# Kernel optimization log

Measured on AMD Instinct MI355X. Metric: run time of the kernel, lower is better.

The kernel has to match this reference:

```python
import jax, jax.numpy as jnp
import numpy as np

N_HEAD = 8


def setup_inputs() -> dict:
    key = jax.random.key(0)
    ks = jax.random.split(key, 8)
    v, b, c, h, w = 8, 4, 512, 16, 16
    s = 1.0 / np.sqrt(c).astype(np.float32)
    return {
        "q": jax.random.normal(ks[0], (v, b, c, h, w), jnp.float32),
        "kv": jax.random.normal(ks[1], (v, b, c, h, w), jnp.float32),
        "Wq": jax.random.normal(ks[2], (c, c), jnp.float32) * s,
        "bq": jnp.zeros((c,), jnp.float32),
        "Wkv": jax.random.normal(ks[3], (c, 2 * c), jnp.float32) * s,
        "bkv": jnp.zeros((2 * c,), jnp.float32),
        "Wp": jax.random.normal(ks[4], (c, c), jnp.float32) * s,
        "bp": jnp.zeros((c,), jnp.float32),
    }


def reference(q, kv, Wq, bq, Wkv, bkv, Wp, bp):
    vi, bi, ci, hi, wi = q.shape
    hw = hi * wi
    T = vi * hw
    hd = ci // N_HEAD

    # rearrange 'v b c h w -> b (v h w) c'
    xq = q.transpose(1, 0, 3, 4, 2).reshape(bi, T, ci)
    xkv = kv.transpose(1, 0, 3, 4, 2).reshape(bi, T, ci)

    qp = xq @ Wq + bq                      # [b, T, c]
    k, v_ = jnp.split(xkv @ Wkv + bkv, 2, axis=-1)

    def heads(x):
        return x.reshape(bi, T, N_HEAD, hd).transpose(0, 2, 1, 3)  # [b,h,T,d]

    qh, kh, vh = heads(qp), heads(k), heads(v_)

    att = jnp.einsum('bhqd,bhkd->bhqk', qh, kh) * (1.0 / np.sqrt(hd).astype(np.float32))

    # block-causal mask: query block (size h*w) may attend to key blocks <= its own
    blocks = jnp.arange(T) // hw
    mask = blocks[:, None] >= blocks[None, :]
    att = jnp.where(mask, att, -jnp.inf)
    att = jax.nn.softmax(att, axis=-1)

    y = jnp.einsum('bhqk,bhkd->bhqd', att, vh)
    y = y.transpose(0, 2, 1, 3).reshape(bi, T, ci)
    y = y @ Wp + bp

    # rearrange 'b (v h w) c -> v b c h w'
    return y.reshape(bi, vi, hi, wi, ci).transpose(1, 0, 4, 2, 3)
```

## Files before the change

### kernel.cpp

```cpp
#include <hip/hip_runtime.h>
#include <hip/hip_bf16.h>
#include <cmath>

typedef unsigned short u16;
typedef __attribute__((ext_vector_type(8))) short s8v;
typedef __attribute__((ext_vector_type(4))) float f4v;
typedef __attribute__((ext_vector_type(2))) float f2v;
typedef __attribute__((ext_vector_type(4))) unsigned int u32x4;
typedef __attribute__((ext_vector_type(4))) unsigned short u16x4;

#define MFMA(a,b,c) __builtin_amdgcn_mfma_f32_16x16x32_bf16((a),(b),(c),0,0,0)

__device__ __forceinline__ float bf2f(u16 u) {
    union { float f; unsigned i; } x; x.i = ((unsigned)u) << 16; return x.f;
}
__device__ __forceinline__ u16 f2bf(float f) {
    union { float f; unsigned i; } x; x.f = f;
    unsigned r = x.i + 0x7FFFu + ((x.i >> 16) & 1u);
    return (u16)(r >> 16);
}
__device__ __forceinline__ unsigned cvtpk(float lo, float hi) {
    unsigned r;
    asm("v_cvt_pk_bf16_f32 %0, %1, %2" : "=v"(r) : "v"(lo), "v"(hi));
    return r;
}
__device__ __forceinline__ void gload_lds16(const void* g, void* l) {
    __builtin_amdgcn_global_load_lds(
        (const __attribute__((address_space(1))) unsigned int*)g,
        (__attribute__((address_space(3))) unsigned int*)l, 16, 0, 0);
}
__device__ __forceinline__ int swb(int row, int colb) {
    return row * 128 + (colb ^ ((((row >> 4) ^ row) & 7) << 4));
}

__constant__ int CPER[8]  = {1,1,2,2,3,3,4,4};
__constant__ int POFF[17] = {0,1,2,3,4,6,8,10,12,15,18,21,24,28,32,36,40};

__global__ __launch_bounds__(256, 3)
void qkv_proj(const float* __restrict__ q, const float* __restrict__ kv,
              const float* __restrict__ Wq, const float* __restrict__ bq,
              const float* __restrict__ Wkv, const float* __restrict__ bkv,
              u16* __restrict__ QH, u16* __restrict__ KH, u16* __restrict__ VT)
{
    __shared__ __align__(16) u16 Tl[2][128 * 64];

    const int bid = blockIdx.x;
    const int x = bid & 7, i = bid >> 3;
    const int mt = x + 8 * (i / 12);
    const int nt = i % 12;
    const int m0 = mt << 7, n0 = nt << 7;

    const int tid  = threadIdx.x;
    const int lane = tid & 63;
    const int w    = tid >> 6;
    const int wr = (w >> 1) * 64, wc = (w & 1) * 64;
    const int cl = lane & 15, rl = lane >> 4;

    const int bb  = m0 >> 11;
    const int t0  = m0 & 2047;
    const int vv  = t0 >> 8;
    const int hw0 = t0 & 255;

    const float* Abase = ((nt < 4) ? q : kv) + (size_t)(vv * 4 + bb) * 131072 + hw0;

    const float* W; const float* bias; int NW, wn0, dn0; u16* dst;
    if (nt < 4)      { W = Wq;  bias = bq;  NW = 512;  wn0 = n0;       dn0 = n0;        dst = QH; }
    else if (nt < 8) { W = Wkv; bias = bkv; NW = 1024; wn0 = n0 - 512; dn0 = n0 - 512;  dst = KH; }
    else             { W = Wkv; bias = bkv; NW = 1024; wn0 = n0 - 512; dn0 = n0 - 1024; dst = VT; }

    const float oscale = (nt < 4) ? 0.18033688011f : 1.0f;

    f4v acc[4][4] = {};
    f2v la0[8], lb0[8], la1[8], lb1[8];

    const int mh = tid & 63;
    const int kb = tid >> 6;

#define QKV_LOAD(dA, dB, k0_) do {                                           \
        const float* gA = Abase + (size_t)((k0_) + kb * 8) * 256 + mh * 2;   \
        const float* gB = W + (size_t)((k0_) + kb * 8) * NW + wn0 + mh * 2;  \
        _Pragma("unroll")                                                    \
        for (int j = 0; j < 8; ++j) {                                        \
            dA[j] = *reinterpret_cast<const f2v*>(gA + j * 256);             \
            dB[j] = *reinterpret_cast<const f2v*>(gB + (size_t)j * NW);      \
        }                                                                    \
    } while (0)

#define QKV_WRITE(bufi, sA, sB) do {                                         \
        _Pragma("unroll")                                                    \
        for (int e = 0; e < 2; ++e) {                                        \
            u32x4 pa, pb;                                                    \
            _Pragma("unroll")                                                \
            for (int jj = 0; jj < 4; ++jj) {                                 \
                pa[jj] = cvtpk(sA[jj * 2][e], sA[jj * 2 + 1][e]);            \
                pb[jj] = cvtpk(sB[jj * 2][e], sB[jj * 2 + 1][e]);            \
            }                                                                \
            *(u32x4*)((char*)&Tl[bufi][0] + swb(mh * 2 + e, kb * 16)) = pa;  \
            *(u32x4*)((char*)&Tl[bufi][0] + swb(mh * 2 + e, 64 + kb * 16)) = pb; \
        }                                                                    \
    } while (0)

#define QKV_MFMA(bufi) do {                                                  \
        s8v af[4], bf[4];                                                    \
        _Pragma("unroll")                                                    \
        for (int mi = 0; mi < 4; ++mi)                                       \
            af[mi] = *(const s8v*)((const char*)&Tl[bufi][0]                 \
                                   + swb(wr + mi * 16 + cl, rl * 16));       \
        _Pragma("unroll")                                                    \
        for (int ni = 0; ni < 4; ++ni)                                       \
            bf[ni] = *(const s8v*)((const char*)&Tl[bufi][0]                 \
                                   + swb(wc + ni * 16 + cl, 64 + rl * 16));  \
        _Pragma("unroll")                                                    \
        for (int mi = 0; mi < 4; ++mi)                                       \
            _Pragma("unroll")                                                \
            for (int ni = 0; ni < 4; ++ni)                                   \
                acc[mi][ni] = MFMA(af[mi], bf[ni], acc[mi][ni]);             \
    } while (0)

    QKV_LOAD(la0, lb0, 0);
    QKV_WRITE(0, la0, lb0);
    QKV_LOAD(la1, lb1, 32);
    __syncthreads();

    #pragma unroll
    for (int it = 0; it < 8; ++it) {
        const int t = it * 2;
        QKV_WRITE(1, la1, lb1);
        if (t + 2 < 16) QKV_LOAD(la0, lb0, (t + 2) * 32);
        QKV_MFMA(0);
        __syncthreads();
        if (t + 2 < 16) QKV_WRITE(0, la0, lb0);
        if (t + 3 < 16) QKV_LOAD(la1, lb1, (t + 3) * 32);
        QKV_MFMA(1);
        __syncthreads();
    }
#undef QKV_LOAD
#undef QKV_WRITE
#undef QKV_MFMA

    if (nt < 8) {
        #pragma unroll
        for (int ni = 0; ni < 4; ++ni) {
            const int nl   = wc + ni * 16 + cl;
            const float bv = bias[wn0 + nl];
            const int cout = dn0 + nl;
            const int hh = cout >> 6, dd = cout & 63;
            const size_t obase = ((size_t)(bb * 8 + hh) * 2048) * 64 + dd;
            #pragma unroll
            for (int mi = 0; mi < 4; ++mi)
                #pragma unroll
                for (int r = 0; r < 4; ++r) {
                    const int m = m0 + wr + mi * 16 + rl * 4 + r;
                    const int t = m & 2047;
                    dst[obase + (size_t)t * 64] = f2bf((acc[mi][ni][r] + bv) * oscale);
                }
        }
    } else {
        #pragma unroll
        for (int ni = 0; ni < 4; ++ni) {
            const int nl   = wc + ni * 16 + cl;
            const float bv = bias[wn0 + nl];
            const int cout = dn0 + nl;
            const int hh = cout >> 6, dd = cout & 63;
            const size_t obase = ((size_t)(bb * 8 + hh) * 64 + dd) * 2048;
            #pragma unroll
            for (int mi = 0; mi < 4; ++mi) {
                const int m = m0 + wr + mi * 16 + rl * 4;
                const int t = m & 2047;
                u16x4 pk;
                #pragma unroll
                for (int r = 0; r < 4; ++r) pk[r] = f2bf(acc[mi][ni][r] + bv);
                *reinterpret_cast<u16x4*>(dst + obase + t) = pk;
            }
        }
    }
}

__global__ __launch_bounds__(256, 4)
void attn_part(const u16* __restrict__ QH, const u16* __restrict__ KH,
               const u16* __restrict__ VT,
               u16* __restrict__ Opart, float* __restrict__ ML)
{
    __shared__ __align__(16) u16 Kl[2][4096];
    __shared__ __align__(16) u16 Vl[2][4096];
    __shared__ u16 Pl[4][16][36];

    const int wg = blockIdx.x;
    const int bh = wg & 31;
    const int s  = 39 - (wg >> 5);
    int p = 0;
    #pragma unroll
    for (int i = 0; i < 15; ++i) p += (s >= POFF[i + 1]) ? 1 : 0;
    const int c  = s - POFF[p];
    const int qb = p >> 1;
    const int kstart = c * 512;
    const int nk = min(512, (qb + 1) * 256 - kstart);
    const int nt64 = nk >> 6;

    const int tid = threadIdx.x, lane = tid & 63, w = tid >> 6;
    const int cl = lane & 15, rl = lane >> 4;

    const u16* Qb = QH + (size_t)bh * 131072;
    const u16* Kb = KH + (size_t)bh * 131072;
    const u16* Vb = VT + (size_t)bh * 131072;

    const int qrow0 = p * 128 + w * 32;

    s8v qf[2][2];
    #pragma unroll
    for (int mi = 0; mi < 2; ++mi)
        #pragma unroll
        for (int kf = 0; kf < 2; ++kf)
            qf[mi][kf] = *reinterpret_cast<const s8v*>(
                Qb + (size_t)(qrow0 + mi * 16 + cl) * 64 + kf * 32 + rl * 8);

    unsigned kofs[2], vofs[2];
    #pragma unroll
    for (int i = 0; i < 2; ++i) {
        const int f = w * 128 + i * 64 + lane;
        const int row = f >> 3;
        kofs[i] = row * 128 + (((f & 7) * 16) ^ ((row & 7) << 4));
        vofs[i] = row * 4096 + (((f & 7) * 16) ^ ((row & 7) << 4));
    }

#define ISSUE(bufi, kb0_) do {                                               \
        const char* kG = (const char*)Kb + (size_t)(kb0_) * 128;             \
        const char* vG = (const char*)Vb + (size_t)(kb0_) * 2;               \
        char* kL = (char*)&Kl[bufi][0] + w * 2048;                           \
        char* vL = (char*)&Vl[bufi][0] + w * 2048;                           \
        _Pragma("unroll")                                                    \
        for (int i_ = 0; i_ < 2; ++i_) {                                     \
            gload_lds16(kG + kofs[i_], kL + i_ * 1024);                      \
            gload_lds16(vG + vofs[i_], vL + i_ * 1024);                      \
        }                                                                    \
    } while (0)

    f4v o[2][4] = {};
    float lp[8] = {0.f, 0.f, 0.f, 0.f, 0.f, 0.f, 0.f, 0.f};

    ISSUE(0, kstart);

    for (int kt = 0; kt < nt64; ++kt) {
        asm volatile("s_waitcnt vmcnt(0)" ::: "memory");
        __builtin_amdgcn_sched_barrier(0);
        __syncthreads();
        if (kt + 1 < nt64) ISSUE((kt + 1) & 1, kstart + (kt + 1) * 64);

        const char* Kbase = (const char*)&Kl[kt & 1][0];
        const char* Vbase = (const char*)&Vl[kt & 1][0];

        f4v sc[2][4] = {};
        #pragma unroll
        for (int ni = 0; ni < 4; ++ni)
            #pragma unroll
            for (int kf = 0; kf < 2; ++kf) {
                const int row = ni * 16 + cl;
                s8v kfr = *reinterpret_cast<const s8v*>(
                    Kbase + row * 128 + ((kf * 64 + rl * 16) ^ ((row & 7) << 4)));
                sc[0][ni] = MFMA(qf[0][kf], kfr, sc[0][ni]);
                sc[1][ni] = MFMA(qf[1][kf], kfr, sc[1][ni]);
            }

        #pragma unroll
        for (int mi = 0; mi < 2; ++mi)
            #pragma unroll
            for (int ni = 0; ni < 4; ++ni)
                #pragma unroll
                for (int r = 0; r < 4; ++r)
                    sc[mi][ni][r] = exp2f(sc[mi][ni][r]);
        #pragma unroll
        for (int mi = 0; mi < 2; ++mi)
            #pragma unroll
            for (int r = 0; r < 4; ++r)
                lp[mi * 4 + r] += sc[mi][0][r] + sc[mi][1][r]
                                + sc[mi][2][r] + sc[mi][3][r];

        #pragma unroll
        for (int kw = 0; kw < 2; ++kw) {
            s8v pf0, pf1;
            #pragma unroll
            for (int jj = 0; jj < 2; ++jj) {
                const int ni = kw * 2 + jj;
                const unsigned w0 = cvtpk(sc[0][ni][0], sc[0][ni][1]);
                const unsigned w1 = cvtpk(sc[0][ni][2], sc[0][ni][3]);
                const int col = jj * 16 + cl;
                Pl[w][rl * 4 + 0][col] = (u16)w0;
                Pl[w][rl * 4 + 1][col] = (u16)(w0 >> 16);
                Pl[w][rl * 4 + 2][col] = (u16)w1;
                Pl[w][rl * 4 + 3][col] = (u16)(w1 >> 16);
            }
            pf0 = *reinterpret_cast<const s8v*>(&Pl[w][cl][rl * 8]);
            #pragma unroll
            for (int jj = 0; jj < 2; ++jj) {
                const int ni = kw * 2 + jj;
                const unsigned w0 = cvtpk(sc[1][ni][0], sc[1][ni][1]);
                const unsigned w1 = cvtpk(sc[1][ni][2], sc[1][ni][3]);
                const int col = jj * 16 + cl;
                Pl[w][rl * 4 + 0][col] = (u16)w0;
                Pl[w][rl * 4 + 1][col] = (u16)(w0 >> 16);
                Pl[w][rl * 4 + 2][col] = (u16)w1;
                Pl[w][rl * 4 + 3][col] = (u16)(w1 >> 16);
            }
            pf1 = *reinterpret_cast<const s8v*>(&Pl[w][cl][rl * 8]);
            #pragma unroll
            for (int di = 0; di < 4; ++di) {
                const int row = di * 16 + cl;
                s8v vf = *reinterpret_cast<const s8v*>(
                    Vbase + row * 128 + ((kw * 64 + rl * 16) ^ ((row & 7) << 4)));
                o[0][di] = MFMA(pf0, vf, o[0][di]);
                o[1][di] = MFMA(pf1, vf, o[1][di]);
            }
        }
    }
#undef ISSUE

    const int slot = bh * 40 + POFF[p] + c;
    #pragma unroll
    for (int mi = 0; mi < 2; ++mi)
        #pragma unroll
        for (int r = 0; r < 4; ++r) {
            const int idx = mi * 4 + r;
            float ls = lp[idx];
            ls += __shfl_xor(ls, 1);
            ls += __shfl_xor(ls, 2);
            ls += __shfl_xor(ls, 4);
            ls += __shfl_xor(ls, 8);
            const float inv = 1.f / ls;
            const int rloc = w * 32 + mi * 16 + rl * 4 + r;
            if (cl == 0) ML[(size_t)slot * 128 + rloc] = ls;
            #pragma unroll
            for (int di = 0; di < 4; ++di)
                Opart[(size_t)slot * 8192 + rloc * 64 + di * 16 + cl] =
                    f2bf(o[mi][di][r] * inv);
        }
}

__global__ __launch_bounds__(256)
void attn_combine(const u16* __restrict__ Opart, const float* __restrict__ ML,
                  u16* __restrict__ YH)
{
    const int wg = blockIdx.x;
    const int bh = wg & 31;
    const int p  = wg >> 5;
    const int b = bh >> 3, h = bh & 7;
    const int nc = CPER[p >> 1];
    const int sb = bh * 40 + POFF[p];

    const int t = threadIdx.x;
    const int rloc = t >> 1;
    const int dh = (t & 1) * 32;

    float lc[4], L = 0.f;
    for (int c = 0; c < nc; ++c) {
        lc[c] = ML[(size_t)(sb + c) * 128 + rloc];
        L += lc[c];
    }
    const float invL = 1.f / L;
    float wgt[4];
    for (int c = 0; c < nc; ++c) wgt[c] = lc[c] * invL;

    f4v a[8] = {};
    for (int c = 0; c < nc; ++c) {
        const float wv = wgt[c];
        #pragma unroll
        for (int u = 0; u < 4; ++u) {
            s8v vv = *reinterpret_cast<const s8v*>(
                &Opart[(size_t)(sb + c) * 8192 + rloc * 64 + dh + u * 8]);
            #pragma unroll
            for (int e = 0; e < 4; ++e) a[u * 2][e]     += wv * bf2f((u16)vv[e]);
            #pragma unroll
            for (int e = 0; e < 4; ++e) a[u * 2 + 1][e] += wv * bf2f((u16)vv[e + 4]);
        }
    }

    const size_t ybase = ((size_t)b * 2048 + p * 128 + rloc) * 512 + h * 64 + dh;
    #pragma unroll
    for (int u = 0; u < 4; ++u) {
        s8v ov;
        #pragma unroll
        for (int e = 0; e < 4; ++e) ov[e]     = (short)f2bf(a[u * 2][e]);
        #pragma unroll
        for (int e = 0; e < 4; ++e) ov[e + 4] = (short)f2bf(a[u * 2 + 1][e]);
        *reinterpret_cast<s8v*>(YH + ybase + u * 8) = ov;
    }
}

__global__ __launch_bounds__(256)
void out_proj(const u16* __restrict__ YH, const float* __restrict__ Wp,
              const float* __restrict__ bp, float* __restrict__ out)
{
    __shared__ __align__(16) u16 Al[2][128 * 64];
    __shared__ u16 Bl[2][128][40];

    const int bid = blockIdx.x;
    const int x = bid & 7, i = bid >> 3;
    const int mt = x + 8 * (i >> 2);
    const int ct = i & 3;
    const int c0 = ct << 7, m0 = mt << 7;

    const int tid = threadIdx.x, lane = tid & 63, w = tid >> 6;
    const int wr = (w >> 1) * 64, wc = (w & 1) * 64;
    const int cl = lane & 15, rl = lane >> 4;

    f4v acc[4][4] = {};
    f2v wa0[8], wa1[8];
    s8v sy0[2], sy1[2];

    const int mh = tid & 63;
    const int kb = tid >> 6;
    const int br = tid >> 2;
    const int bq4 = (tid & 3) * 8;

#define OP_LOAD(dA, dY, k0_) do {                                            \
        const float* gA = Wp + (size_t)((k0_) + kb * 8) * 512 + c0 + mh * 2; \
        _Pragma("unroll")                                                    \
        for (int j = 0; j < 8; ++j)                                          \
            dA[j] = *reinterpret_cast<const f2v*>(gA + j * 512);             \
        _Pragma("unroll")                                                    \
        for (int it = 0; it < 2; ++it)                                       \
            dY[it] = *reinterpret_cast<const s8v*>(                          \
                YH + (size_t)(m0 + br + it * 64) * 512 + (k0_) + bq4);       \
    } while (0)

#define OP_WRITE(bufi, sA, sY) do {                                          \
        _Pragma("unroll")                                                    \
        for (int e = 0; e < 2; ++e) {                                        \
            u32x4 pa;                                                        \
            _Pragma("unroll")                                                \
            for (int jj = 0; jj < 4; ++jj)                                   \
                pa[jj] = cvtpk(sA[jj * 2][e], sA[jj * 2 + 1][e]);            \
            *(u32x4*)((char*)&Al[bufi][0] + swb(mh * 2 + e, kb * 16)) = pa;  \
        }                                                                    \
        _Pragma("unroll")                                                    \
        for (int it = 0; it < 2; ++it)                                       \
            *reinterpret_cast<s8v*>(&Bl[bufi][br + it * 64][bq4]) = sY[it];  \
    } while (0)

#define OP_MFMA(bufi) do {                                                   \
        s8v af[4], bfr[4];                                                   \
        _Pragma("unroll")                                                    \
        for (int mi = 0; mi < 4; ++mi)                                       \
            af[mi] = *(const s8v*)((const char*)&Al[bufi][0]                 \
                                   + swb(wr + mi * 16 + cl, rl * 16));       \
        _Pragma("unroll")                                                    \
        for (int ni = 0; ni < 4; ++ni)                                       \
            bfr[ni] = *reinterpret_cast<const s8v*>(                         \
                &Bl[bufi][wc + ni * 16 + cl][rl * 8]);                       \
        _Pragma("unroll")                                                    \
        for (int mi = 0; mi < 4; ++mi)                                       \
            _Pragma("unroll")                                                \
            for (int ni = 0; ni < 4; ++ni)                                   \
                acc[mi][ni] = MFMA(af[mi], bfr[ni], acc[mi][ni]);            \
    } while (0)

    OP_LOAD(wa0, sy0, 0);
    OP_WRITE(0, wa0, sy0);
    OP_LOAD(wa1, sy1, 32);
    __syncthreads();

    #pragma unroll
    for (int it = 0; it < 8; ++it) {
        const int t = it * 2;
        OP_WRITE(1, wa1, sy1);
        if (t + 2 < 16) OP_LOAD(wa0, sy0, (t + 2) * 32);
        OP_MFMA(0);
        __syncthreads();
        if (t + 2 < 16) OP_WRITE(0, wa0, sy0);
        if (t + 3 < 16) OP_LOAD(wa1, sy1, (t + 3) * 32);
        OP_MFMA(1);
        __syncthreads();
    }
#undef OP_LOAD
#undef OP_WRITE
#undef OP_MFMA

    #pragma unroll
    for (int mi = 0; mi < 4; ++mi)
        #pragma unroll
        for (int r = 0; r < 4; ++r) {
            const int c = c0 + wr + mi * 16 + rl * 4 + r;
            const float bv = bp[c];
            #pragma unroll
            for (int ni = 0; ni < 4; ++ni) {
                const int tok = m0 + wc + ni * 16 + cl;
                const int bb = tok >> 11, t = tok & 2047;
                const int vv = t >> 8, hw = t & 255;
                out[(size_t)(vv * 4 + bb) * 131072 + (size_t)c * 256 + hw] =
                    acc[mi][ni][r] + bv;
            }
        }
}

extern "C" void kernel_launch(void* const* d_in, const int* in_sizes, int n_in,
                              void* d_out, int out_size, void* d_ws, size_t ws_size,
                              hipStream_t stream)
{
    const float* q   = (const float*)d_in[0];
    const float* kv  = (const float*)d_in[1];
    const float* Wq  = (const float*)d_in[2];
    const float* bq  = (const float*)d_in[3];
    const float* Wkv = (const float*)d_in[4];
    const float* bkv = (const float*)d_in[5];
    const float* Wp  = (const float*)d_in[6];
    const float* bp  = (const float*)d_in[7];
    float* out = (float*)d_out;

    u16* ws = (u16*)d_ws;
    u16* QH = ws;
    u16* KH = QH + 4194304;
    u16* VT = KH + 4194304;
    u16* YH = VT + 4194304;
    u16* Opart = YH + 4194304;
    float* ML  = (float*)(Opart + 10485760);

    hipLaunchKernelGGL(qkv_proj, dim3(768), dim3(256), 0, stream,
                       q, kv, Wq, bq, Wkv, bkv, QH, KH, VT);
    hipLaunchKernelGGL(attn_part, dim3(1280), dim3(256), 0, stream,
                       QH, KH, VT, Opart, ML);
    hipLaunchKernelGGL(attn_combine, dim3(512), dim3(256), 0, stream,
                       Opart, ML, YH);
    hipLaunchKernelGGL(out_proj, dim3(256), dim3(256), 0, stream, YH, Wp, bp, out);
}
```

Before: 104.1 us.

## Triple-buffer attention K/V loads and relax GEMM barriers to LDS-only waits

The attention kernel moves from double to triple-buffered K/V tiles in shared memory. It prefetches two tiles ahead and waits with vmcnt(4), so one tile's async loads stay in flight while the current tile is processed. The QKV and output projection GEMMs replace __syncthreads with a barrier that waits only on LDS counters, and they issue the next global loads before the LDS writes so global latency is not drained at each barrier. This raises LDS use in the attention kernel, which may lower occupancy, and the vmcnt ordering has to be exactly right or the kernel reads stale data.

```diff
diff --git a/kernel.cpp b/kernel.cpp
--- a/kernel.cpp
+++ b/kernel.cpp
@@ -28,6 +28,11 @@
     __builtin_amdgcn_global_load_lds(
         (const __attribute__((address_space(1))) unsigned int*)g,
         (__attribute__((address_space(3))) unsigned int*)l, 16, 0, 0);
+}
+__device__ __forceinline__ void lgkm_bar() {
+    asm volatile("s_waitcnt lgkmcnt(0)" ::: "memory");
+    __builtin_amdgcn_sched_barrier(0);
+    __builtin_amdgcn_s_barrier();
 }
 __device__ __forceinline__ int swb(int row, int colb) {
     return row * 128 + (colb ^ ((((row >> 4) ^ row) & 7) << 4));
@@ -120,19 +125,19 @@
     QKV_LOAD(la0, lb0, 0);
     QKV_WRITE(0, la0, lb0);
     QKV_LOAD(la1, lb1, 32);
-    __syncthreads();
+    lgkm_bar();
 
     #pragma unroll
     for (int it = 0; it < 8; ++it) {
         const int t = it * 2;
+        if (t + 2 < 16) QKV_LOAD(la0, lb0, (t + 2) * 32);
         QKV_WRITE(1, la1, lb1);
-        if (t + 2 < 16) QKV_LOAD(la0, lb0, (t + 2) * 32);
         QKV_MFMA(0);
-        __syncthreads();
+        lgkm_bar();
+        if (t + 3 < 16) QKV_LOAD(la1, lb1, (t + 3) * 32);
         if (t + 2 < 16) QKV_WRITE(0, la0, lb0);
-        if (t + 3 < 16) QKV_LOAD(la1, lb1, (t + 3) * 32);
         QKV_MFMA(1);
-        __syncthreads();
+        lgkm_bar();
     }
 #undef QKV_LOAD
 #undef QKV_WRITE
@@ -181,8 +186,8 @@
                const u16* __restrict__ VT,
                u16* __restrict__ Opart, float* __restrict__ ML)
 {
-    __shared__ __align__(16) u16 Kl[2][4096];
-    __shared__ __align__(16) u16 Vl[2][4096];
+    __shared__ __align__(16) u16 Kl[3][4096];
+    __shared__ __align__(16) u16 Vl[3][4096];
     __shared__ u16 Pl[4][16][36];
 
     const int wg = blockIdx.x;
@@ -239,15 +244,18 @@
     float lp[8] = {0.f, 0.f, 0.f, 0.f, 0.f, 0.f, 0.f, 0.f};
 
     ISSUE(0, kstart);
+    ISSUE(1, kstart + 64);
 
     for (int kt = 0; kt < nt64; ++kt) {
-        asm volatile("s_waitcnt vmcnt(0)" ::: "memory");
+        if (kt + 1 < nt64) asm volatile("s_waitcnt vmcnt(4)" ::: "memory");
+        else               asm volatile("s_waitcnt vmcnt(0)" ::: "memory");
         __builtin_amdgcn_sched_barrier(0);
-        __syncthreads();
-        if (kt + 1 < nt64) ISSUE((kt + 1) & 1, kstart + (kt + 1) * 64);
-
-        const char* Kbase = (const char*)&Kl[kt & 1][0];
-        const char* Vbase = (const char*)&Vl[kt & 1][0];
+        __builtin_amdgcn_s_barrier();
+        if (kt + 2 < nt64) ISSUE((kt + 2) % 3, kstart + (kt + 2) * 64);
+
+        const int bi = kt % 3;
+        const char* Kbase = (const char*)&Kl[bi][0];
+        const char* Vbase = (const char*)&Vl[bi][0];
 
         f4v sc[2][4] = {};
         #pragma unroll
@@ -456,19 +464,19 @@
     OP_LOAD(wa0, sy0, 0);
     OP_WRITE(0, wa0, sy0);
     OP_LOAD(wa1, sy1, 32);
-    __syncthreads();
+    lgkm_bar();
 
     #pragma unroll
     for (int it = 0; it < 8; ++it) {
         const int t = it * 2;
+        if (t + 2 < 16) OP_LOAD(wa0, sy0, (t + 2) * 32);
         OP_WRITE(1, wa1, sy1);
-        if (t + 2 < 16) OP_LOAD(wa0, sy0, (t + 2) * 32);
         OP_MFMA(0);
-        __syncthreads();
+        lgkm_bar();
+        if (t + 3 < 16) OP_LOAD(wa1, sy1, (t + 3) * 32);
         if (t + 2 < 16) OP_WRITE(0, wa0, sy0);
-        if (t + 3 < 16) OP_LOAD(wa1, sy1, (t + 3) * 32);
         OP_MFMA(1);
-        __syncthreads();
+        lgkm_bar();
     }
 #undef OP_LOAD
 #undef OP_WRITE
```

New measurement: 107.4 us, median of 2. +3.1%, slower.

## Fuse split-KV combine into output projection and relax LDS barriers

Applied to the files above, without the earlier changes.

Removes the attn_combine kernel and its YH intermediate. out_proj now computes per-row combine weights from ML into shared memory, then loads the partial outputs directly and reduces them into the B-operand tile while staging. The __syncthreads calls in qkv_proj and out_proj become a custom lgkmcnt wait plus s_barrier, and global loads are issued before the LDS writes. This saves a launch and a full global round trip, at the cost of more global loads and ALU work inside the GEMM mainloop and weaker barrier semantics.

```diff
diff --git a/kernel.cpp b/kernel.cpp
--- a/kernel.cpp
+++ b/kernel.cpp
@@ -28,6 +28,11 @@
     __builtin_amdgcn_global_load_lds(
         (const __attribute__((address_space(1))) unsigned int*)g,
         (__attribute__((address_space(3))) unsigned int*)l, 16, 0, 0);
+}
+__device__ __forceinline__ void lgkm_bar() {
+    asm volatile("s_waitcnt lgkmcnt(0)" ::: "memory");
+    __builtin_amdgcn_sched_barrier(0);
+    __builtin_amdgcn_s_barrier();
 }
 __device__ __forceinline__ int swb(int row, int colb) {
     return row * 128 + (colb ^ ((((row >> 4) ^ row) & 7) << 4));
@@ -120,19 +125,19 @@
     QKV_LOAD(la0, lb0, 0);
     QKV_WRITE(0, la0, lb0);
     QKV_LOAD(la1, lb1, 32);
-    __syncthreads();
+    lgkm_bar();
 
     #pragma unroll
     for (int it = 0; it < 8; ++it) {
         const int t = it * 2;
+        if (t + 2 < 16) QKV_LOAD(la0, lb0, (t + 2) * 32);
         QKV_WRITE(1, la1, lb1);
-        if (t + 2 < 16) QKV_LOAD(la0, lb0, (t + 2) * 32);
         QKV_MFMA(0);
-        __syncthreads();
+        lgkm_bar();
+        if (t + 3 < 16) QKV_LOAD(la1, lb1, (t + 3) * 32);
         if (t + 2 < 16) QKV_WRITE(0, la0, lb0);
-        if (t + 3 < 16) QKV_LOAD(la1, lb1, (t + 3) * 32);
         QKV_MFMA(1);
-        __syncthreads();
+        lgkm_bar();
     }
 #undef QKV_LOAD
 #undef QKV_WRITE
@@ -336,61 +341,13 @@
 }
 
 __global__ __launch_bounds__(256)
-void attn_combine(const u16* __restrict__ Opart, const float* __restrict__ ML,
-                  u16* __restrict__ YH)
-{
-    const int wg = blockIdx.x;
-    const int bh = wg & 31;
-    const int p  = wg >> 5;
-    const int b = bh >> 3, h = bh & 7;
-    const int nc = CPER[p >> 1];
-    const int sb = bh * 40 + POFF[p];
-
-    const int t = threadIdx.x;
-    const int rloc = t >> 1;
-    const int dh = (t & 1) * 32;
-
-    float lc[4], L = 0.f;
-    for (int c = 0; c < nc; ++c) {
-        lc[c] = ML[(size_t)(sb + c) * 128 + rloc];
-        L += lc[c];
-    }
-    const float invL = 1.f / L;
-    float wgt[4];
-    for (int c = 0; c < nc; ++c) wgt[c] = lc[c] * invL;
-
-    f4v a[8] = {};
-    for (int c = 0; c < nc; ++c) {
-        const float wv = wgt[c];
-        #pragma unroll
-        for (int u = 0; u < 4; ++u) {
-            s8v vv = *reinterpret_cast<const s8v*>(
-                &Opart[(size_t)(sb + c) * 8192 + rloc * 64 + dh + u * 8]);
-            #pragma unroll
-            for (int e = 0; e < 4; ++e) a[u * 2][e]     += wv * bf2f((u16)vv[e]);
-            #pragma unroll
-            for (int e = 0; e < 4; ++e) a[u * 2 + 1][e] += wv * bf2f((u16)vv[e + 4]);
-        }
-    }
-
-    const size_t ybase = ((size_t)b * 2048 + p * 128 + rloc) * 512 + h * 64 + dh;
-    #pragma unroll
-    for (int u = 0; u < 4; ++u) {
-        s8v ov;
-        #pragma unroll
-        for (int e = 0; e < 4; ++e) ov[e]     = (short)f2bf(a[u * 2][e]);
-        #pragma unroll
-        for (int e = 0; e < 4; ++e) ov[e + 4] = (short)f2bf(a[u * 2 + 1][e]);
-        *reinterpret_cast<s8v*>(YH + ybase + u * 8) = ov;
-    }
-}
-
-__global__ __launch_bounds__(256)
-void out_proj(const u16* __restrict__ YH, const float* __restrict__ Wp,
-              const float* __restrict__ bp, float* __restrict__ out)
+void out_proj(const u16* __restrict__ Opart, const float* __restrict__ ML,
+              const float* __restrict__ Wp, const float* __restrict__ bp,
+              float* __restrict__ out)
 {
     __shared__ __align__(16) u16 Al[2][128 * 64];
     __shared__ u16 Bl[2][128][40];
+    __shared__ float Wl[8][128][4];
 
     const int bid = blockIdx.x;
     const int x = bid & 7, i = bid >> 3;
@@ -402,27 +359,56 @@
     const int wr = (w >> 1) * 64, wc = (w & 1) * 64;
     const int cl = lane & 15, rl = lane >> 4;
 
+    const int b = m0 >> 11;
+    const int p = (m0 & 2047) >> 7;
+    const int nc = CPER[p >> 1];
+    const int poff = POFF[p];
+
+    #pragma unroll
+    for (int j = 0; j < 4; ++j) {
+        const int item = tid + 256 * j;
+        const int hh = item >> 7, tk = item & 127;
+        const int sb = (b * 8 + hh) * 40 + poff;
+        float lc[4] = {0.f, 0.f, 0.f, 0.f};
+        float L = 0.f;
+        #pragma unroll
+        for (int c2 = 0; c2 < 4; ++c2)
+            if (c2 < nc) { lc[c2] = ML[(size_t)(sb + c2) * 128 + tk]; L += lc[c2]; }
+        const float invL = 1.f / L;
+        #pragma unroll
+        for (int c2 = 0; c2 < 4; ++c2)
+            Wl[hh][tk][c2] = lc[c2] * invL;
+    }
+
     f4v acc[4][4] = {};
     f2v wa0[8], wa1[8];
-    s8v sy0[2], sy1[2];
+    s8v yr0[2][4], yr1[2][4];
 
     const int mh = tid & 63;
     const int kb = tid >> 6;
     const int br = tid >> 2;
     const int bq4 = (tid & 3) * 8;
 
-#define OP_LOAD(dA, dY, k0_) do {                                            \
+#define OP_LOAD(dA, yr, k0_) do {                                            \
         const float* gA = Wp + (size_t)((k0_) + kb * 8) * 512 + c0 + mh * 2; \
         _Pragma("unroll")                                                    \
         for (int j = 0; j < 8; ++j)                                          \
             dA[j] = *reinterpret_cast<const f2v*>(gA + j * 512);             \
-        _Pragma("unroll")                                                    \
-        for (int it = 0; it < 2; ++it)                                       \
-            dY[it] = *reinterpret_cast<const s8v*>(                          \
-                YH + (size_t)(m0 + br + it * 64) * 512 + (k0_) + bq4);       \
-    } while (0)
-
-#define OP_WRITE(bufi, sA, sY) do {                                          \
+        const int hh_ = (k0_) >> 6;                                          \
+        const int d0_ = ((k0_) & 32) + bq4;                                  \
+        const int sb_ = (b * 8 + hh_) * 40 + poff;                           \
+        _Pragma("unroll")                                                    \
+        for (int it_ = 0; it_ < 2; ++it_) {                                  \
+            const int row_ = br + it_ * 64;                                  \
+            _Pragma("unroll")                                                \
+            for (int c2 = 0; c2 < 4; ++c2)                                   \
+                if (c2 < nc)                                                 \
+                    yr[it_][c2] = *reinterpret_cast<const s8v*>(             \
+                        Opart + (size_t)(sb_ + c2) * 8192 + row_ * 64 + d0_);\
+        }                                                                    \
+    } while (0)
+
+#define OP_WRITE(bufi, sA, yr, k0_) do {                                     \
         _Pragma("unroll")                                                    \
         for (int e = 0; e < 2; ++e) {                                        \
             u32x4 pa;                                                        \
@@ -431,9 +417,32 @@
                 pa[jj] = cvtpk(sA[jj * 2][e], sA[jj * 2 + 1][e]);            \
             *(u32x4*)((char*)&Al[bufi][0] + swb(mh * 2 + e, kb * 16)) = pa;  \
         }                                                                    \
-        _Pragma("unroll")                                                    \
-        for (int it = 0; it < 2; ++it)                                       \
-            *reinterpret_cast<s8v*>(&Bl[bufi][br + it * 64][bq4]) = sY[it];  \
+        const int hh_ = (k0_) >> 6;                                          \
+        _Pragma("unroll")                                                    \
+        for (int it_ = 0; it_ < 2; ++it_) {                                  \
+            const int row_ = br + it_ * 64;                                  \
+            f4v y0 = {0.f,0.f,0.f,0.f}, y1 = {0.f,0.f,0.f,0.f};              \
+            _Pragma("unroll")                                                \
+            for (int c2 = 0; c2 < 4; ++c2)                                   \
+                if (c2 < nc) {                                               \
+                    const float wv = Wl[hh_][row_][c2];                      \
+                    _Pragma("unroll")                                        \
+                    for (int e2 = 0; e2 < 4; ++e2) {                         \
+                        y0[e2] += wv * bf2f((u16)yr[it_][c2][e2]);           \
+                        y1[e2] += wv * bf2f((u16)yr[it_][c2][e2 + 4]);       \
+                    }                                                        \
+                }                                                            \
+            s8v sy;                                                          \
+            unsigned p0 = cvtpk(y0[0], y0[1]);                               \
+            unsigned p1 = cvtpk(y0[2], y0[3]);                               \
+            unsigned p2 = cvtpk(y1[0], y1[1]);                               \
+            unsigned p3 = cvtpk(y1[2], y1[3]);                               \
+            sy[0] = (short)(u16)p0; sy[1] = (short)(u16)(p0 >> 16);          \
+            sy[2] = (short)(u16)p1; sy[3] = (short)(u16)(p1 >> 16);          \
+            sy[4] = (short)(u16)p2; sy[5] = (short)(u16)(p2 >> 16);          \
+            sy[6] = (short)(u16)p3; sy[7] = (short)(u16)(p3 >> 16);          \
+            *reinterpret_cast<s8v*>(&Bl[bufi][row_][bq4]) = sy;              \
+        }                                                                    \
     } while (0)
 
 #define OP_MFMA(bufi) do {                                                   \
@@ -453,22 +462,23 @@
                 acc[mi][ni] = MFMA(af[mi], bfr[ni], acc[mi][ni]);            \
     } while (0)
 
-    OP_LOAD(wa0, sy0, 0);
-    OP_WRITE(0, wa0, sy0);
-    OP_LOAD(wa1, sy1, 32);
-    __syncthreads();
+    OP_LOAD(wa0, yr0, 0);
+    lgkm_bar();
+    OP_WRITE(0, wa0, yr0, 0);
+    OP_LOAD(wa1, yr1, 32);
+    lgkm_bar();
 
     #pragma unroll
     for (int it = 0; it < 8; ++it) {
         const int t = it * 2;
-        OP_WRITE(1, wa1, sy1);
-        if (t + 2 < 16) OP_LOAD(wa0, sy0, (t + 2) * 32);
+        if (t + 2 < 16) OP_LOAD(wa0, yr0, (t + 2) * 32);
+        OP_WRITE(1, wa1, yr1, (t + 1) * 32);
         OP_MFMA(0);
-        __syncthreads();
-        if (t + 2 < 16) OP_WRITE(0, wa0, sy0);
-        if (t + 3 < 16) OP_LOAD(wa1, sy1, (t + 3) * 32);
+        lgkm_bar();
+        if (t + 3 < 16) OP_LOAD(wa1, yr1, (t + 3) * 32);
+        if (t + 2 < 16) OP_WRITE(0, wa0, yr0, (t + 2) * 32);
         OP_MFMA(1);
-        __syncthreads();
+        lgkm_bar();
     }
 #undef OP_LOAD
 #undef OP_WRITE
@@ -509,15 +519,13 @@
     u16* QH = ws;
     u16* KH = QH + 4194304;
     u16* VT = KH + 4194304;
-    u16* YH = VT + 4194304;
-    u16* Opart = YH + 4194304;
+    u16* Opart = VT + 4194304;
     float* ML  = (float*)(Opart + 10485760);
 
     hipLaunchKernelGGL(qkv_proj, dim3(768), dim3(256), 0, stream,
                        q, kv, Wq, bq, Wkv, bkv, QH, KH, VT);
     hipLaunchKernelGGL(attn_part, dim3(1280), dim3(256), 0, stream,
                        QH, KH, VT, Opart, ML);
-    hipLaunchKernelGGL(attn_combine, dim3(512), dim3(256), 0, stream,
-                       Opart, ML, YH);
-    hipLaunchKernelGGL(out_proj, dim3(256), dim3(256), 0, stream, YH, Wp, bp, out);
-}
+    hipLaunchKernelGGL(out_proj, dim3(256), dim3(256), 0, stream,
+                       Opart, ML, Wp, bp, out);
+}
```

Result: slower. 107.6 us (+3.4%).

## Process two 64-key tiles per iteration with four-deep K/V LDS buffering

Applied to the files above, without the earlier changes.

The attention loop now handles two 64-key tiles per iteration, issuing both score MFMA chains together and prefetching the next two tiles into a four-slot LDS ring. This halves the number of barriers and vmcnt waits and exposes more independent MFMA work per wave. The cost is doubled LDS and register use, so the launch bound drops from 4 to 2 blocks per CU, which lowers occupancy. The code assumes nt64 is even, which holds because nk is a multiple of 256.

```diff
diff --git a/kernel.cpp b/kernel.cpp
--- a/kernel.cpp
+++ b/kernel.cpp
@@ -176,14 +176,14 @@
     }
 }
 
-__global__ __launch_bounds__(256, 4)
+__global__ __launch_bounds__(256, 2)
 void attn_part(const u16* __restrict__ QH, const u16* __restrict__ KH,
                const u16* __restrict__ VT,
                u16* __restrict__ Opart, float* __restrict__ ML)
 {
-    __shared__ __align__(16) u16 Kl[2][4096];
-    __shared__ __align__(16) u16 Vl[2][4096];
-    __shared__ u16 Pl[4][16][36];
+    __shared__ __align__(16) u16 Kl[4][4096];
+    __shared__ __align__(16) u16 Vl[4][4096];
+    __shared__ u16 Pl[2][4][16][36];
 
     const int wg = blockIdx.x;
     const int bh = wg & 31;
@@ -239,26 +239,35 @@
     float lp[8] = {0.f, 0.f, 0.f, 0.f, 0.f, 0.f, 0.f, 0.f};
 
     ISSUE(0, kstart);
-
-    for (int kt = 0; kt < nt64; ++kt) {
+    ISSUE(1, kstart + 64);
+
+    for (int kt = 0; kt < nt64; kt += 2) {
         asm volatile("s_waitcnt vmcnt(0)" ::: "memory");
         __builtin_amdgcn_sched_barrier(0);
         __syncthreads();
-        if (kt + 1 < nt64) ISSUE((kt + 1) & 1, kstart + (kt + 1) * 64);
-
-        const char* Kbase = (const char*)&Kl[kt & 1][0];
-        const char* Vbase = (const char*)&Vl[kt & 1][0];
-
-        f4v sc[2][4] = {};
+        if (kt + 3 < nt64) {
+            ISSUE((kt + 2) & 3, kstart + (kt + 2) * 64);
+            ISSUE((kt + 3) & 3, kstart + (kt + 3) * 64);
+        }
+
+        const char* KbA = (const char*)&Kl[kt & 3][0];
+        const char* VbA = (const char*)&Vl[kt & 3][0];
+        const char* KbB = (const char*)&Kl[(kt + 1) & 3][0];
+        const char* VbB = (const char*)&Vl[(kt + 1) & 3][0];
+
+        f4v scA[2][4] = {}, scB[2][4] = {};
         #pragma unroll
         for (int ni = 0; ni < 4; ++ni)
             #pragma unroll
             for (int kf = 0; kf < 2; ++kf) {
                 const int row = ni * 16 + cl;
-                s8v kfr = *reinterpret_cast<const s8v*>(
-                    Kbase + row * 128 + ((kf * 64 + rl * 16) ^ ((row & 7) << 4)));
-                sc[0][ni] = MFMA(qf[0][kf], kfr, sc[0][ni]);
-                sc[1][ni] = MFMA(qf[1][kf], kfr, sc[1][ni]);
+                const int off = (kf * 64 + rl * 16) ^ ((row & 7) << 4);
+                s8v kfrA = *reinterpret_cast<const s8v*>(KbA + row * 128 + off);
+                s8v kfrB = *reinterpret_cast<const s8v*>(KbB + row * 128 + off);
+                scA[0][ni] = MFMA(qf[0][kf], kfrA, scA[0][ni]);
+                scA[1][ni] = MFMA(qf[1][kf], kfrA, scA[1][ni]);
+                scB[0][ni] = MFMA(qf[0][kf], kfrB, scB[0][ni]);
+                scB[1][ni] = MFMA(qf[1][kf], kfrB, scB[1][ni]);
             }
 
         #pragma unroll
@@ -266,49 +275,58 @@
             #pragma unroll
             for (int ni = 0; ni < 4; ++ni)
                 #pragma unroll
-                for (int r = 0; r < 4; ++r)
-                    sc[mi][ni][r] = exp2f(sc[mi][ni][r]);
+                for (int r = 0; r < 4; ++r) {
+                    scA[mi][ni][r] = exp2f(scA[mi][ni][r]);
+                    scB[mi][ni][r] = exp2f(scB[mi][ni][r]);
+                }
         #pragma unroll
         for (int mi = 0; mi < 2; ++mi)
             #pragma unroll
             for (int r = 0; r < 4; ++r)
-                lp[mi * 4 + r] += sc[mi][0][r] + sc[mi][1][r]
-                                + sc[mi][2][r] + sc[mi][3][r];
-
-        #pragma unroll
-        for (int kw = 0; kw < 2; ++kw) {
-            s8v pf0, pf1;
-            #pragma unroll
-            for (int jj = 0; jj < 2; ++jj) {
-                const int ni = kw * 2 + jj;
-                const unsigned w0 = cvtpk(sc[0][ni][0], sc[0][ni][1]);
-                const unsigned w1 = cvtpk(sc[0][ni][2], sc[0][ni][3]);
-                const int col = jj * 16 + cl;
-                Pl[w][rl * 4 + 0][col] = (u16)w0;
-                Pl[w][rl * 4 + 1][col] = (u16)(w0 >> 16);
-                Pl[w][rl * 4 + 2][col] = (u16)w1;
-                Pl[w][rl * 4 + 3][col] = (u16)(w1 >> 16);
-            }
-            pf0 = *reinterpret_cast<const s8v*>(&Pl[w][cl][rl * 8]);
-            #pragma unroll
-            for (int jj = 0; jj < 2; ++jj) {
-                const int ni = kw * 2 + jj;
-                const unsigned w0 = cvtpk(sc[1][ni][0], sc[1][ni][1]);
-                const unsigned w1 = cvtpk(sc[1][ni][2], sc[1][ni][3]);
-                const int col = jj * 16 + cl;
-                Pl[w][rl * 4 + 0][col] = (u16)w0;
-                Pl[w][rl * 4 + 1][col] = (u16)(w0 >> 16);
-                Pl[w][rl * 4 + 2][col] = (u16)w1;
-                Pl[w][rl * 4 + 3][col] = (u16)(w1 >> 16);
-            }
-            pf1 = *reinterpret_cast<const s8v*>(&Pl[w][cl][rl * 8]);
-            #pragma unroll
-            for (int di = 0; di < 4; ++di) {
-                const int row = di * 16 + cl;
-                s8v vf = *reinterpret_cast<const s8v*>(
-                    Vbase + row * 128 + ((kw * 64 + rl * 16) ^ ((row & 7) << 4)));
-                o[0][di] = MFMA(pf0, vf, o[0][di]);
-                o[1][di] = MFMA(pf1, vf, o[1][di]);
+                lp[mi * 4 + r] += scA[mi][0][r] + scA[mi][1][r]
+                                + scA[mi][2][r] + scA[mi][3][r]
+                                + scB[mi][0][r] + scB[mi][1][r]
+                                + scB[mi][2][r] + scB[mi][3][r];
+
+        #pragma unroll
+        for (int tb = 0; tb < 2; ++tb) {
+            f4v (*sc)[4] = tb ? scB : scA;
+            const char* Vbase = tb ? VbB : VbA;
+            #pragma unroll
+            for (int kw = 0; kw < 2; ++kw) {
+                s8v pf0, pf1;
+                #pragma unroll
+                for (int jj = 0; jj < 2; ++jj) {
+                    const int ni = kw * 2 + jj;
+                    const unsigned w0 = cvtpk(sc[0][ni][0], sc[0][ni][1]);
+                    const unsigned w1 = cvtpk(sc[0][ni][2], sc[0][ni][3]);
+                    const int col = jj * 16 + cl;
+                    Pl[tb][w][rl * 4 + 0][col] = (u16)w0;
+                    Pl[tb][w][rl * 4 + 1][col] = (u16)(w0 >> 16);
+                    Pl[tb][w][rl * 4 + 2][col] = (u16)w1;
+                    Pl[tb][w][rl * 4 + 3][col] = (u16)(w1 >> 16);
+                }
+                pf0 = *reinterpret_cast<const s8v*>(&Pl[tb][w][cl][rl * 8]);
+                #pragma unroll
+                for (int jj = 0; jj < 2; ++jj) {
+                    const int ni = kw * 2 + jj;
+                    const unsigned w0 = cvtpk(sc[1][ni][0], sc[1][ni][1]);
+                    const unsigned w1 = cvtpk(sc[1][ni][2], sc[1][ni][3]);
+                    const int col = jj * 16 + cl;
+                    Pl[tb][w][rl * 4 + 0][col] = (u16)w0;
+                    Pl[tb][w][rl * 4 + 1][col] = (u16)(w0 >> 16);
+                    Pl[tb][w][rl * 4 + 2][col] = (u16)w1;
+                    Pl[tb][w][rl * 4 + 3][col] = (u16)(w1 >> 16);
+                }
+                pf1 = *reinterpret_cast<const s8v*>(&Pl[tb][w][cl][rl * 8]);
+                #pragma unroll
+                for (int di = 0; di < 4; ++di) {
+                    const int row = di * 16 + cl;
+                    s8v vf = *reinterpret_cast<const s8v*>(
+                        Vbase + row * 128 + ((kw * 64 + rl * 16) ^ ((row & 7) << 4)));
+                    o[0][di] = MFMA(pf0, vf, o[0][di]);
+                    o[1][di] = MFMA(pf1, vf, o[1][di]);
+                }
             }
         }
     }
```

Measured after the change: 106.4 us. 2.1% more time.
